# Optimization experiments

Measured on AMD Instinct MI355X. Metric: run time of the kernel, lower is better.

The kernel has to match this reference:

```python
import jax, jax.numpy as jnp
import numpy as np

N = 100000   # nodes
E = 625000   # edges
D = 128      # feature / embedding dim
C = 40       # num classes
BN_EPS = 1e-5
L2_EPS = 1e-12


def setup_inputs() -> dict:
    key = jax.random.key(0)
    ks = jax.random.split(key, 8)
    s = 1.0 / np.sqrt(D)
    return {
        "x": jax.random.normal(ks[0], (N, D), dtype=jnp.float32),
        "edge_index": jax.random.randint(ks[1], (2, E), 0, N, dtype=jnp.int64),
        "W1": jax.random.normal(ks[2], (D, D), dtype=jnp.float32) * s,
        "b1": jnp.zeros((D,), jnp.float32),
        "W2": jax.random.normal(ks[3], (D, D), dtype=jnp.float32) * s,
        "b2": jnp.zeros((D,), jnp.float32),
        "W3": jax.random.normal(ks[4], (D, D), dtype=jnp.float32) * s,
        "b3": jnp.zeros((D,), jnp.float32),
        "g1": jnp.ones((D,), jnp.float32), "be1": jnp.zeros((D,), jnp.float32),
        "g2": jnp.ones((D,), jnp.float32), "be2": jnp.zeros((D,), jnp.float32),
        "g3": jnp.ones((D,), jnp.float32), "be3": jnp.zeros((D,), jnp.float32),
        "Wout": jax.random.normal(ks[5], (D, C), dtype=jnp.float32) * s,
        "bout": jnp.zeros((C,), jnp.float32),
    }


def _gcn_norm(edge_index, n):
    # PyG GCNConv default: add self loops, symmetric normalization
    loop = jnp.arange(n)
    src = jnp.concatenate([edge_index[0], loop])
    dst = jnp.concatenate([edge_index[1], loop])
    deg = jax.ops.segment_sum(jnp.ones_like(src, dtype=jnp.float32), dst, num_segments=n)
    dinv = jnp.where(deg > 0, jax.lax.rsqrt(deg), 0.0)
    norm = dinv[src] * dinv[dst]  # [E+N]
    return src, dst, norm


def _gcn_conv(x, W, b, src, dst, norm, n):
    h = x @ W                                # [N, D]
    msg = h[src] * norm[:, None]             # gather, [E+N, D]
    out = jax.ops.segment_sum(msg, dst, num_segments=n)  # scatter-add
    return out + b


def _bn(x, g, b):
    mu = jnp.mean(x, axis=0)
    var = jnp.var(x, axis=0)
    return (x - mu) * jax.lax.rsqrt(var + BN_EPS) * g + b


def _l2norm(x):
    n = jnp.sqrt(jnp.sum(x * x, axis=1, keepdims=True))
    return x / jnp.maximum(n, L2_EPS)


def reference(x, edge_index, W1, b1, W2, b2, W3, b3,
              g1, be1, g2, be2, g3, be3, Wout, bout):
    n = x.shape[0]
    src, dst, norm = _gcn_norm(edge_index, n)

    h = jax.nn.relu(_bn(_gcn_conv(x, W1, b1, src, dst, norm, n), g1, be1))
    h = _l2norm(h)
    r = h
    h = jax.nn.relu(_bn(_gcn_conv(h, W2, b2, src, dst, norm, n), g2, be2))
    h = _l2norm(h + r)
    r = h
    h = jax.nn.relu(_bn(_gcn_conv(h, W3, b3, src, dst, norm, n), g3, be3))
    h = _l2norm(h + r)

    return h @ Wout + bout  # node classification logits [N, C]
```

## Files before the change

kernel.cpp:

```cpp
#include <hip/hip_runtime.h>
#include <math.h>

#define DD 128
#define COUT 40
#define BN_EPS 1e-5f
#define L2_EPS 1e-12f
#define NREP 64

typedef __attribute__((ext_vector_type(8))) short bf16x8;
typedef __attribute__((ext_vector_type(4))) float f32x4;

static __device__ inline unsigned short f2bf(float f) {
    unsigned int x = __float_as_uint(f);
    unsigned int r = (x + 0x7FFFu + ((x >> 16) & 1u)) >> 16;
    return (unsigned short)r;
}
static __device__ inline float bf2f(unsigned short u) {
    return __uint_as_float(((unsigned int)u) << 16);
}


__global__ void k_hist(const int* __restrict__ ei, int E, int* __restrict__ deg,
                       int* __restrict__ pord) {
    int i = blockIdx.x * blockDim.x + threadIdx.x;
    if (i < E) pord[i] = atomicAdd(&deg[ei[E + i]], 1);
}

__global__ void k_scan_a(const int* __restrict__ deg, int* __restrict__ row_ptr,
                         int* __restrict__ bsum, float* __restrict__ dinv, int n) {
    __shared__ int s[256];
    int t = threadIdx.x;
    int idx = blockIdx.x * 256 + t;
    int v = (idx < n) ? deg[idx] + 1 : 0;
    if (idx < n) dinv[idx] = rsqrtf((float)v);
    s[t] = v; __syncthreads();
    for (int off = 1; off < 256; off <<= 1) {
        int x = (t >= off) ? s[t - off] : 0;
        __syncthreads(); s[t] += x; __syncthreads();
    }
    if (idx <= n) row_ptr[idx] = s[t] - v;
    if (t == 255) bsum[blockIdx.x] = s[255];
}

__global__ void k_scan_b(const int* __restrict__ bsum, int* __restrict__ boff, int nb) {
    __shared__ int s[512];
    int t = threadIdx.x;
    int v = (t < nb) ? bsum[t] : 0;
    s[t] = v; __syncthreads();
    for (int off = 1; off < 512; off <<= 1) {
        int x = (t >= off) ? s[t - off] : 0;
        __syncthreads(); s[t] += x; __syncthreads();
    }
    if (t < nb) boff[t] = s[t] - v;
}

__global__ void k_scan_c(int* __restrict__ row_ptr, const int* __restrict__ boff, int n1) {
    int idx = blockIdx.x * blockDim.x + threadIdx.x;
    if (idx < n1) row_ptr[idx] += boff[idx >> 8];
}

__global__ void k_fill(const int* __restrict__ ei, const int* __restrict__ pord,
                       int E, int n, const int* __restrict__ row_ptr,
                       int* __restrict__ perm) {
    int i = blockIdx.x * blockDim.x + threadIdx.x;
    int total = E + n;
    if (i >= total) return;
    int u, pos;
    if (i < E) {
        u = ei[i];
        int v = ei[E + i];
        pos = row_ptr[v] + pord[i];
    } else {
        u = i - E;
        pos = row_ptr[u + 1] - 1;
    }
    perm[pos] = u;
}

__global__ void k_wrepack_all(const float* __restrict__ W1, const float* __restrict__ W2,
                              const float* __restrict__ W3, const float* __restrict__ Wout,
                              unsigned short* __restrict__ wb,
                              unsigned short* __restrict__ wob,
                              float* __restrict__ stats) {
    int b = blockIdx.x;
    if (b < 24) {
        int wi = b >> 3;
        const float* W = (wi == 0) ? W1 : (wi == 1) ? W2 : W3;
        unsigned short* out = wb + wi * 16384;
        int idx = (b & 7) * 256 + threadIdx.x;
        int kc = idx >> 9;
        int cc = (idx >> 6) & 7;
        int lane = idx & 63;
        int n = cc * 16 + (lane & 15);
        int kb = kc * 32 + (lane >> 4) * 8;
        unsigned short tmp[8];
#pragma unroll
        for (int j = 0; j < 8; j++) tmp[j] = f2bf(W[(size_t)(kb + j) * DD + n]);
        *(uint4*)&out[(size_t)idx * 8] = *(const uint4*)tmp;
    } else if (b < 27) {
        int idx = (b - 24) * 256 + threadIdx.x;
        int kc = idx / 192;
        int rem = idx % 192;
        int cc = rem >> 6;
        int lane = rem & 63;
        int n = cc * 16 + (lane & 15);
        int kb = kc * 32 + (lane >> 4) * 8;
        unsigned short tmp[8];
#pragma unroll
        for (int j = 0; j < 8; j++)
            tmp[j] = (n < COUT) ? f2bf(Wout[(size_t)(kb + j) * COUT + n]) : 0;
        *(uint4*)&wob[(size_t)idx * 8] = *(const uint4*)tmp;
    } else {
        float4 z = make_float4(0.f, 0.f, 0.f, 0.f);
        int idx = (b - 27) * 256 + threadIdx.x;
        for (int i = idx; i < 3 * NREP * 64; i += 8 * 256)
            ((float4*)stats)[i] = z;
    }
}


__global__ __launch_bounds__(256) void k_gemm0(const float* __restrict__ A,
                                               const unsigned short* __restrict__ Wb,
                                               const float* __restrict__ dinv,
                                               unsigned short* __restrict__ C, int nrows) {
    __shared__ __align__(16) unsigned short Ws[16384];
    const int tid = threadIdx.x;
    for (int i = tid; i < 2048; i += 256)
        ((uint4*)Ws)[i] = ((const uint4*)Wb)[i];
    __syncthreads();

    const int wv = tid >> 6;
    const int lane = tid & 63;
    const int R0 = blockIdx.x * 64 + wv * 16;
    if (R0 >= nrows) return;
    const int m = lane & 15, q = lane >> 4;
    int rr = R0 + m; if (rr >= nrows) rr = nrows - 1;
    const float* Ar = A + (size_t)rr * DD + q * 8;

    bf16x8 af[4];
#pragma unroll
    for (int kc = 0; kc < 4; kc++) {
        float4 lo = *(const float4*)(Ar + kc * 32);
        float4 hi = *(const float4*)(Ar + kc * 32 + 4);
        unsigned short t[8];
        t[0] = f2bf(lo.x); t[1] = f2bf(lo.y); t[2] = f2bf(lo.z); t[3] = f2bf(lo.w);
        t[4] = f2bf(hi.x); t[5] = f2bf(hi.y); t[6] = f2bf(hi.z); t[7] = f2bf(hi.w);
        af[kc] = *(const bf16x8*)t;
    }

    f32x4 acc[8];
#pragma unroll
    for (int cc = 0; cc < 8; cc++) acc[cc] = (f32x4){0.f, 0.f, 0.f, 0.f};
#pragma unroll
    for (int kc = 0; kc < 4; kc++)
#pragma unroll
        for (int cc = 0; cc < 8; cc++) {
            bf16x8 b = *(const bf16x8*)&Ws[(size_t)((kc * 8 + cc) * 64 + lane) * 8];
            acc[cc] = __builtin_amdgcn_mfma_f32_16x16x32_bf16(af[kc], b, acc[cc], 0, 0, 0);
        }

    float dr[4];
#pragma unroll
    for (int i = 0; i < 4; i++) {
        int r = R0 + q * 4 + i;
        dr[i] = (r < nrows) ? dinv[r] : 0.f;
    }
#pragma unroll
    for (int cc = 0; cc < 8; cc++)
#pragma unroll
        for (int i = 0; i < 4; i++) {
            int r = R0 + q * 4 + i;
            if (r < nrows) C[(size_t)r * DD + cc * 16 + m] = f2bf(acc[cc][i] * dr[i]);
        }
}

__global__ __launch_bounds__(256) void k_aggs(const unsigned short* __restrict__ lin,
                                              const int* __restrict__ row_ptr,
                                              const int* __restrict__ perm,
                                              const float* __restrict__ dinv,
                                              const float* __restrict__ bias,
                                              unsigned short* __restrict__ outb,
                                              float* __restrict__ stats, int n) {
    const int tid = threadIdx.x;
    const int wv = tid >> 6;
    const int lane = tid & 63;
    const int half = lane >> 5;
    const int li = lane & 31;
    const int slot = li >> 4;
    const int ci = (li & 15) * 8;

    const int v = blockIdx.x * 8 + wv * 2 + half;
    const bool valid = v < n;

    float acc[8];
#pragma unroll
    for (int k = 0; k < 8; k++) acc[k] = 0.f;
    float dv = 0.f;

    if (valid) {
        const int s0 = row_ptr[v];
        const int e0 = row_ptr[v + 1];
        dv = dinv[v];
        for (int j = s0; j < e0; j += 8) {
            int i0 = j + slot;
            int i1 = j + 2 + slot;
            int i2 = j + 4 + slot;
            int i3 = j + 6 + slot;
            bool b0 = i0 < e0, b1 = i1 < e0, b2 = i2 < e0, b3 = i3 < e0;
            int u0, u1, u2, u3;
            if (b0) u0 = perm[i0];
            if (b1) u1 = perm[i1];
            if (b2) u2 = perm[i2];
            if (b3) u3 = perm[i3];
            uint4 t0, t1, t2, t3;
            if (b0) t0 = *(const uint4*)&lin[(size_t)u0 * DD + ci];
            if (b1) t1 = *(const uint4*)&lin[(size_t)u1 * DD + ci];
            if (b2) t2 = *(const uint4*)&lin[(size_t)u2 * DD + ci];
            if (b3) t3 = *(const uint4*)&lin[(size_t)u3 * DD + ci];
            if (b0) {
                acc[0] += __uint_as_float(t0.x << 16);
                acc[1] += __uint_as_float(t0.x & 0xFFFF0000u);
                acc[2] += __uint_as_float(t0.y << 16);
                acc[3] += __uint_as_float(t0.y & 0xFFFF0000u);
                acc[4] += __uint_as_float(t0.z << 16);
                acc[5] += __uint_as_float(t0.z & 0xFFFF0000u);
                acc[6] += __uint_as_float(t0.w << 16);
                acc[7] += __uint_as_float(t0.w & 0xFFFF0000u);
            }
            if (b1) {
                acc[0] += __uint_as_float(t1.x << 16);
                acc[1] += __uint_as_float(t1.x & 0xFFFF0000u);
                acc[2] += __uint_as_float(t1.y << 16);
                acc[3] += __uint_as_float(t1.y & 0xFFFF0000u);
                acc[4] += __uint_as_float(t1.z << 16);
                acc[5] += __uint_as_float(t1.z & 0xFFFF0000u);
                acc[6] += __uint_as_float(t1.w << 16);
                acc[7] += __uint_as_float(t1.w & 0xFFFF0000u);
            }
            if (b2) {
                acc[0] += __uint_as_float(t2.x << 16);
                acc[1] += __uint_as_float(t2.x & 0xFFFF0000u);
                acc[2] += __uint_as_float(t2.y << 16);
                acc[3] += __uint_as_float(t2.y & 0xFFFF0000u);
                acc[4] += __uint_as_float(t2.z << 16);
                acc[5] += __uint_as_float(t2.z & 0xFFFF0000u);
                acc[6] += __uint_as_float(t2.w << 16);
                acc[7] += __uint_as_float(t2.w & 0xFFFF0000u);
            }
            if (b3) {
                acc[0] += __uint_as_float(t3.x << 16);
                acc[1] += __uint_as_float(t3.x & 0xFFFF0000u);
                acc[2] += __uint_as_float(t3.y << 16);
                acc[3] += __uint_as_float(t3.y & 0xFFFF0000u);
                acc[4] += __uint_as_float(t3.z << 16);
                acc[5] += __uint_as_float(t3.z & 0xFFFF0000u);
                acc[6] += __uint_as_float(t3.w << 16);
                acc[7] += __uint_as_float(t3.w & 0xFFFF0000u);
            }
        }
    }
#pragma unroll
    for (int k = 0; k < 8; k++) acc[k] += __shfl_xor(acc[k], 16, 64);

    __shared__ float sh[8][128];
    __shared__ float qh[8][128];
    const int prow = wv * 2 + half;
    if (slot == 0) {
        if (valid) {
            float4 bb0 = *(const float4*)&bias[ci];
            float4 bb1 = *(const float4*)&bias[ci + 4];
            float bs[8] = {bb0.x, bb0.y, bb0.z, bb0.w, bb1.x, bb1.y, bb1.z, bb1.w};
            unsigned short t[8];
#pragma unroll
            for (int k = 0; k < 8; k++) {
                float a = acc[k] * dv + bs[k];
                t[k] = f2bf(a);
                sh[prow][ci + k] = a;
                qh[prow][ci + k] = a * a;
            }
            *(uint4*)&outb[(size_t)v * DD + ci] = *(const uint4*)t;
        } else {
#pragma unroll
            for (int k = 0; k < 8; k++) { sh[prow][ci + k] = 0.f; qh[prow][ci + k] = 0.f; }
        }
    }
    __syncthreads();
    if (tid < 128) {
        float a = 0.f, b = 0.f;
#pragma unroll
        for (int g = 0; g < 8; g++) { a += sh[g][tid]; b += qh[g][tid]; }
        float* st = stats + (size_t)(blockIdx.x & (NREP - 1)) * 256;
        atomicAdd(&st[tid], a);
        atomicAdd(&st[128 + tid], b);
    }
}

template <bool HAS_RES>
__global__ __launch_bounds__(256) void k_fused(const unsigned short* __restrict__ aggX,
                                               const float* __restrict__ stats,
                                               const float* __restrict__ g,
                                               const float* __restrict__ be, float inv_n,
                                               const unsigned short* __restrict__ resb,
                                               const unsigned short* __restrict__ Wb,
                                               const float* __restrict__ dinv,
                                               unsigned short* __restrict__ hbf_out,
                                               unsigned short* __restrict__ linb_out,
                                               int nrows) {
    __shared__ __align__(16) unsigned short Ws[16384];
    __shared__ float ssl[256];
    const int tid = threadIdx.x;
    for (int i = tid; i < 2048; i += 256)
        ((uint4*)Ws)[i] = ((const uint4*)Wb)[i];
    if (tid < 128) {
        float sa = 0.f, sb = 0.f;
        for (int r = 0; r < NREP; r++) {
            sa += stats[r * 256 + tid];
            sb += stats[r * 256 + 128 + tid];
        }
        float mu = sa * inv_n;
        float var = sb * inv_n - mu * mu;
        float sc = g[tid] * rsqrtf(var + BN_EPS);
        ssl[tid] = sc;
        ssl[128 + tid] = be[tid] - mu * sc;
    }
    __syncthreads();

    const int wv = tid >> 6;
    const int lane = tid & 63;
    const int R0 = blockIdx.x * 64 + wv * 16;
    if (R0 >= nrows) return;
    const int m = lane & 15, q = lane >> 4;
    int rr = R0 + m; if (rr >= nrows) rr = nrows - 1;
    const unsigned short* Ar = aggX + (size_t)rr * DD + q * 8;
    const unsigned short* Rr = HAS_RES ? resb + (size_t)rr * DD + q * 8 : nullptr;

    float y[4][8];
    float sq = 0.f;
#pragma unroll
    for (int kc = 0; kc < 4; kc++) {
        ushort4 lo = *(const ushort4*)(Ar + kc * 32);
        ushort4 hi = *(const ushort4*)(Ar + kc * 32 + 4);
        unsigned short av[8] = {lo.x, lo.y, lo.z, lo.w, hi.x, hi.y, hi.z, hi.w};
        int c0 = kc * 32 + q * 8;
        float4 sc0 = *(const float4*)&ssl[c0];
        float4 sc1 = *(const float4*)&ssl[c0 + 4];
        float4 sh0 = *(const float4*)&ssl[128 + c0];
        float4 sh1 = *(const float4*)&ssl[128 + c0 + 4];
        float scv[8] = {sc0.x, sc0.y, sc0.z, sc0.w, sc1.x, sc1.y, sc1.z, sc1.w};
        float shv[8] = {sh0.x, sh0.y, sh0.z, sh0.w, sh1.x, sh1.y, sh1.z, sh1.w};
        if (HAS_RES) {
            ushort4 rl = *(const ushort4*)(Rr + kc * 32);
            ushort4 rh = *(const ushort4*)(Rr + kc * 32 + 4);
            unsigned short rv[8] = {rl.x, rl.y, rl.z, rl.w, rh.x, rh.y, rh.z, rh.w};
#pragma unroll
            for (int j = 0; j < 8; j++) {
                float yy = fmaxf(bf2f(av[j]) * scv[j] + shv[j], 0.f) + bf2f(rv[j]);
                y[kc][j] = yy; sq += yy * yy;
            }
        } else {
#pragma unroll
            for (int j = 0; j < 8; j++) {
                float yy = fmaxf(bf2f(av[j]) * scv[j] + shv[j], 0.f);
                y[kc][j] = yy; sq += yy * yy;
            }
        }
    }
    sq += __shfl_xor(sq, 16, 64);
    sq += __shfl_xor(sq, 32, 64);
    float inv = 1.f / fmaxf(sqrtf(sq), L2_EPS);

    bf16x8 af[4];
#pragma unroll
    for (int kc = 0; kc < 4; kc++) {
        unsigned short t[8];
#pragma unroll
        for (int j = 0; j < 8; j++) t[j] = f2bf(y[kc][j] * inv);
        af[kc] = *(const bf16x8*)t;
        *(bf16x8*)&hbf_out[(size_t)rr * DD + q * 8 + kc * 32] = af[kc];
    }

    f32x4 acc[8];
#pragma unroll
    for (int cc = 0; cc < 8; cc++) acc[cc] = (f32x4){0.f, 0.f, 0.f, 0.f};
#pragma unroll
    for (int kc = 0; kc < 4; kc++)
#pragma unroll
        for (int cc = 0; cc < 8; cc++) {
            bf16x8 b = *(const bf16x8*)&Ws[(size_t)((kc * 8 + cc) * 64 + lane) * 8];
            acc[cc] = __builtin_amdgcn_mfma_f32_16x16x32_bf16(af[kc], b, acc[cc], 0, 0, 0);
        }

    float dr[4];
#pragma unroll
    for (int i = 0; i < 4; i++) {
        int r = R0 + q * 4 + i;
        dr[i] = (r < nrows) ? dinv[r] : 0.f;
    }
#pragma unroll
    for (int cc = 0; cc < 8; cc++)
#pragma unroll
        for (int i = 0; i < 4; i++) {
            int r = R0 + q * 4 + i;
            if (r < nrows) linb_out[(size_t)r * DD + cc * 16 + m] = f2bf(acc[cc][i] * dr[i]);
        }
}

__global__ __launch_bounds__(256) void k_outfused(const unsigned short* __restrict__ aggX,
                                                  const float* __restrict__ stats,
                                                  const float* __restrict__ g,
                                                  const float* __restrict__ be, float inv_n,
                                                  const unsigned short* __restrict__ resb,
                                                  const unsigned short* __restrict__ wob,
                                                  const float* __restrict__ bout,
                                                  float* __restrict__ C, int nrows) {
    __shared__ __align__(16) unsigned short Ws[6144];
    __shared__ float ssl[256];
    const int tid = threadIdx.x;
    for (int i = tid; i < 768; i += 256)
        ((uint4*)Ws)[i] = ((const uint4*)wob)[i];
    if (tid < 128) {
        float sa = 0.f, sb = 0.f;
        for (int r = 0; r < NREP; r++) {
            sa += stats[r * 256 + tid];
            sb += stats[r * 256 + 128 + tid];
        }
        float mu = sa * inv_n;
        float var = sb * inv_n - mu * mu;
        float sc = g[tid] * rsqrtf(var + BN_EPS);
        ssl[tid] = sc;
        ssl[128 + tid] = be[tid] - mu * sc;
    }
    __syncthreads();

    const int wv = tid >> 6;
    const int lane = tid & 63;
    const int R0 = blockIdx.x * 64 + wv * 16;
    if (R0 >= nrows) return;
    const int m = lane & 15, q = lane >> 4;
    int rr = R0 + m; if (rr >= nrows) rr = nrows - 1;
    const unsigned short* Ar = aggX + (size_t)rr * DD + q * 8;
    const unsigned short* Rr = resb + (size_t)rr * DD + q * 8;

    float y[4][8];
    float sq = 0.f;
#pragma unroll
    for (int kc = 0; kc < 4; kc++) {
        ushort4 lo = *(const ushort4*)(Ar + kc * 32);
        ushort4 hi = *(const ushort4*)(Ar + kc * 32 + 4);
        ushort4 rl = *(const ushort4*)(Rr + kc * 32);
        ushort4 rh = *(const ushort4*)(Rr + kc * 32 + 4);
        unsigned short av[8] = {lo.x, lo.y, lo.z, lo.w, hi.x, hi.y, hi.z, hi.w};
        unsigned short rv[8] = {rl.x, rl.y, rl.z, rl.w, rh.x, rh.y, rh.z, rh.w};
        int c0 = kc * 32 + q * 8;
        float4 sc0 = *(const float4*)&ssl[c0];
        float4 sc1 = *(const float4*)&ssl[c0 + 4];
        float4 sh0 = *(const float4*)&ssl[128 + c0];
        float4 sh1 = *(const float4*)&ssl[128 + c0 + 4];
        float scv[8] = {sc0.x, sc0.y, sc0.z, sc0.w, sc1.x, sc1.y, sc1.z, sc1.w};
        float shv[8] = {sh0.x, sh0.y, sh0.z, sh0.w, sh1.x, sh1.y, sh1.z, sh1.w};
#pragma unroll
        for (int j = 0; j < 8; j++) {
            float yy = fmaxf(bf2f(av[j]) * scv[j] + shv[j], 0.f) + bf2f(rv[j]);
            y[kc][j] = yy; sq += yy * yy;
        }
    }
    sq += __shfl_xor(sq, 16, 64);
    sq += __shfl_xor(sq, 32, 64);
    float inv = 1.f / fmaxf(sqrtf(sq), L2_EPS);

    bf16x8 af[4];
#pragma unroll
    for (int kc = 0; kc < 4; kc++) {
        unsigned short t[8];
#pragma unroll
        for (int j = 0; j < 8; j++) t[j] = f2bf(y[kc][j] * inv);
        af[kc] = *(const bf16x8*)t;
    }

    f32x4 acc[3];
#pragma unroll
    for (int cc = 0; cc < 3; cc++) acc[cc] = (f32x4){0.f, 0.f, 0.f, 0.f};
#pragma unroll
    for (int kc = 0; kc < 4; kc++)
#pragma unroll
        for (int cc = 0; cc < 3; cc++) {
            bf16x8 b = *(const bf16x8*)&Ws[(size_t)((kc * 3 + cc) * 64 + lane) * 8];
            acc[cc] = __builtin_amdgcn_mfma_f32_16x16x32_bf16(af[kc], b, acc[cc], 0, 0, 0);
        }

#pragma unroll
    for (int cc = 0; cc < 3; cc++) {
        int col = cc * 16 + m;
        if (col < COUT) {
            float bb = bout[col];
#pragma unroll
            for (int i = 0; i < 4; i++) {
                int r = R0 + q * 4 + i;
                if (r < nrows) C[(size_t)r * COUT + col] = acc[cc][i] + bb;
            }
        }
    }
}


extern "C" void kernel_launch(void* const* d_in, const int* in_sizes, int n_in,
                              void* d_out, int out_size, void* d_ws, size_t ws_size,
                              hipStream_t stream) {
    const float* x    = (const float*)d_in[0];
    const int*   ei   = (const int*)d_in[1];
    const float* W1   = (const float*)d_in[2];
    const float* b1   = (const float*)d_in[3];
    const float* W2   = (const float*)d_in[4];
    const float* b2   = (const float*)d_in[5];
    const float* W3   = (const float*)d_in[6];
    const float* b3   = (const float*)d_in[7];
    const float* g1   = (const float*)d_in[8];
    const float* be1  = (const float*)d_in[9];
    const float* g2   = (const float*)d_in[10];
    const float* be2  = (const float*)d_in[11];
    const float* g3   = (const float*)d_in[12];
    const float* be3  = (const float*)d_in[13];
    const float* Wout = (const float*)d_in[14];
    const float* bout = (const float*)d_in[15];
    float* out = (float*)d_out;

    const int N = in_sizes[0] / DD;
    const int E = in_sizes[1] / 2;
    const int NNZ = E + N;
    const int SSTRIDE = NREP * 256;

    char* w = (char*)d_ws;
    unsigned short* linb = (unsigned short*)w; w += (size_t)N * DD * sizeof(unsigned short);
    unsigned short* aggA = (unsigned short*)w; w += (size_t)N * DD * sizeof(unsigned short);
    unsigned short* aggB = (unsigned short*)w; w += (size_t)N * DD * sizeof(unsigned short);
    unsigned short* hbf1 = (unsigned short*)w; w += (size_t)N * DD * sizeof(unsigned short);
    unsigned short* hbf2 = (unsigned short*)w; w += (size_t)N * DD * sizeof(unsigned short);
    unsigned short* wb   = (unsigned short*)w; w += 3 * 16384 * sizeof(unsigned short);
    unsigned short* wob  = (unsigned short*)w; w += 6144 * sizeof(unsigned short);
    int* perm    = (int*)w;                    w += (size_t)NNZ * sizeof(int);
    int* pord    = (int*)w;                    w += (size_t)E * sizeof(int);
    int* deg     = (int*)w;                    w += (size_t)N * sizeof(int);
    int* row_ptr = (int*)w;                    w += (size_t)(N + 1) * sizeof(int);
    float* dinv  = (float*)w;                  w += (size_t)N * sizeof(float);
    int* bsum    = (int*)w;                    w += 512 * sizeof(int);
    int* boff    = (int*)w;                    w += 512 * sizeof(int);
    float* stats = (float*)w;                  w += 3 * (size_t)SSTRIDE * sizeof(float);

    const int NB = (N + 1 + 255) / 256;

    hipMemsetAsync(deg, 0, (size_t)N * sizeof(int), stream);
    k_wrepack_all<<<35, 256, 0, stream>>>(W1, W2, W3, Wout, wb, wob, stats);
    k_hist<<<(E + 255) / 256, 256, 0, stream>>>(ei, E, deg, pord);
    k_scan_a<<<NB, 256, 0, stream>>>(deg, row_ptr, bsum, dinv, N);
    k_scan_b<<<1, 512, 0, stream>>>(bsum, boff, NB);
    k_scan_c<<<(N + 1 + 255) / 256, 256, 0, stream>>>(row_ptr, boff, N + 1);
    k_fill<<<(NNZ + 255) / 256, 256, 0, stream>>>(ei, pord, E, N, row_ptr, perm);

    int gemmGrid = (N + 63) / 64;
    int aggGrid = (N + 7) / 8;
    float inv_n = 1.0f / (float)N;

    k_gemm0<<<gemmGrid, 256, 0, stream>>>(x, wb, dinv, linb, N);
    k_aggs<<<aggGrid, 256, 0, stream>>>(linb, row_ptr, perm, dinv, b1, aggA, stats, N);
    k_fused<false><<<gemmGrid, 256, 0, stream>>>(aggA, stats, g1, be1, inv_n,
                                                 nullptr, wb + 16384, dinv, hbf1, linb, N);
    k_aggs<<<aggGrid, 256, 0, stream>>>(linb, row_ptr, perm, dinv, b2, aggB,
                                        stats + SSTRIDE, N);
    k_fused<true><<<gemmGrid, 256, 0, stream>>>(aggB, stats + SSTRIDE, g2, be2, inv_n,
                                                hbf1, wb + 32768, dinv, hbf2, linb, N);
    k_aggs<<<aggGrid, 256, 0, stream>>>(linb, row_ptr, perm, dinv, b3, aggA,
                                        stats + 2 * SSTRIDE, N);
    k_outfused<<<gemmGrid, 256, 0, stream>>>(aggA, stats + 2 * SSTRIDE, g3, be3, inv_n,
                                             hbf2, wob, bout, out, N);
}
```

Measured before the change: 404.5 us.

## Shard aggregation over feature columns with 16-lane groups per node

The SpMM aggregation kernel now splits the 128 feature columns into 8 shards handled by separate blocks. Each block covers 16 nodes, and each 16-lane group works on one node's 16-column slice, with 8 edge slots of 2 lanes each, reduced by shuffles. The aim is more parallelism per node and a simpler edge loop. In exchange, every block re-reads row_ptr and perm for its shard, and each gather is only 32 bytes per lane pair. Nontemporal loads and stores are also added for perm and the aggregation output.

```diff
diff --git a/kernel.cpp b/kernel.cpp
--- a/kernel.cpp
+++ b/kernel.cpp
@@ -9,6 +9,7 @@
 
 typedef __attribute__((ext_vector_type(8))) short bf16x8;
 typedef __attribute__((ext_vector_type(4))) float f32x4;
+typedef __attribute__((ext_vector_type(4))) unsigned int u32x4;
 
 static __device__ inline unsigned short f2bf(float f) {
     unsigned int x = __float_as_uint(f);
@@ -74,7 +75,7 @@
         u = i - E;
         pos = row_ptr[u + 1] - 1;
     }
-    perm[pos] = u;
+    __builtin_nontemporal_store(u, &perm[pos]);
 }
 
 __global__ void k_wrepack_all(const float* __restrict__ W1, const float* __restrict__ W2,
@@ -182,14 +183,15 @@
                                               unsigned short* __restrict__ outb,
                                               float* __restrict__ stats, int n) {
     const int tid = threadIdx.x;
-    const int wv = tid >> 6;
-    const int lane = tid & 63;
-    const int half = lane >> 5;
-    const int li = lane & 31;
-    const int slot = li >> 4;
-    const int ci = (li & 15) * 8;
-
-    const int v = blockIdx.x * 8 + wv * 2 + half;
+    const int shard = blockIdx.x & 7;
+    const int bg = blockIdx.x >> 3;
+    const int grp = tid >> 4;
+    const int li = tid & 15;
+    const int slot = li >> 1;
+    const int lp = li & 1;
+    const int c0 = shard * 16 + lp * 8;
+
+    const int v = bg * 16 + grp;
     const bool valid = v < n;
 
     float acc[8];
@@ -201,97 +203,56 @@
         const int s0 = row_ptr[v];
         const int e0 = row_ptr[v + 1];
         dv = dinv[v];
-        for (int j = s0; j < e0; j += 8) {
-            int i0 = j + slot;
-            int i1 = j + 2 + slot;
-            int i2 = j + 4 + slot;
-            int i3 = j + 6 + slot;
-            bool b0 = i0 < e0, b1 = i1 < e0, b2 = i2 < e0, b3 = i3 < e0;
-            int u0, u1, u2, u3;
-            if (b0) u0 = perm[i0];
-            if (b1) u1 = perm[i1];
-            if (b2) u2 = perm[i2];
-            if (b3) u3 = perm[i3];
-            uint4 t0, t1, t2, t3;
-            if (b0) t0 = *(const uint4*)&lin[(size_t)u0 * DD + ci];
-            if (b1) t1 = *(const uint4*)&lin[(size_t)u1 * DD + ci];
-            if (b2) t2 = *(const uint4*)&lin[(size_t)u2 * DD + ci];
-            if (b3) t3 = *(const uint4*)&lin[(size_t)u3 * DD + ci];
-            if (b0) {
-                acc[0] += __uint_as_float(t0.x << 16);
-                acc[1] += __uint_as_float(t0.x & 0xFFFF0000u);
-                acc[2] += __uint_as_float(t0.y << 16);
-                acc[3] += __uint_as_float(t0.y & 0xFFFF0000u);
-                acc[4] += __uint_as_float(t0.z << 16);
-                acc[5] += __uint_as_float(t0.z & 0xFFFF0000u);
-                acc[6] += __uint_as_float(t0.w << 16);
-                acc[7] += __uint_as_float(t0.w & 0xFFFF0000u);
-            }
-            if (b1) {
-                acc[0] += __uint_as_float(t1.x << 16);
-                acc[1] += __uint_as_float(t1.x & 0xFFFF0000u);
-                acc[2] += __uint_as_float(t1.y << 16);
-                acc[3] += __uint_as_float(t1.y & 0xFFFF0000u);
-                acc[4] += __uint_as_float(t1.z << 16);
-                acc[5] += __uint_as_float(t1.z & 0xFFFF0000u);
-                acc[6] += __uint_as_float(t1.w << 16);
-                acc[7] += __uint_as_float(t1.w & 0xFFFF0000u);
-            }
-            if (b2) {
-                acc[0] += __uint_as_float(t2.x << 16);
-                acc[1] += __uint_as_float(t2.x & 0xFFFF0000u);
-                acc[2] += __uint_as_float(t2.y << 16);
-                acc[3] += __uint_as_float(t2.y & 0xFFFF0000u);
-                acc[4] += __uint_as_float(t2.z << 16);
-                acc[5] += __uint_as_float(t2.z & 0xFFFF0000u);
-                acc[6] += __uint_as_float(t2.w << 16);
-                acc[7] += __uint_as_float(t2.w & 0xFFFF0000u);
-            }
-            if (b3) {
-                acc[0] += __uint_as_float(t3.x << 16);
-                acc[1] += __uint_as_float(t3.x & 0xFFFF0000u);
-                acc[2] += __uint_as_float(t3.y << 16);
-                acc[3] += __uint_as_float(t3.y & 0xFFFF0000u);
-                acc[4] += __uint_as_float(t3.z << 16);
-                acc[5] += __uint_as_float(t3.z & 0xFFFF0000u);
-                acc[6] += __uint_as_float(t3.w << 16);
-                acc[7] += __uint_as_float(t3.w & 0xFFFF0000u);
-            }
-        }
-    }
-#pragma unroll
-    for (int k = 0; k < 8; k++) acc[k] += __shfl_xor(acc[k], 16, 64);
-
-    __shared__ float sh[8][128];
-    __shared__ float qh[8][128];
-    const int prow = wv * 2 + half;
-    if (slot == 0) {
+        for (int j = s0 + slot; j < e0; j += 8) {
+            int u = __builtin_nontemporal_load(&perm[j]);
+            u32x4 t = *(const u32x4*)&lin[(size_t)u * DD + c0];
+            acc[0] += __uint_as_float(t[0] << 16);
+            acc[1] += __uint_as_float(t[0] & 0xFFFF0000u);
+            acc[2] += __uint_as_float(t[1] << 16);
+            acc[3] += __uint_as_float(t[1] & 0xFFFF0000u);
+            acc[4] += __uint_as_float(t[2] << 16);
+            acc[5] += __uint_as_float(t[2] & 0xFFFF0000u);
+            acc[6] += __uint_as_float(t[3] << 16);
+            acc[7] += __uint_as_float(t[3] & 0xFFFF0000u);
+        }
+    }
+#pragma unroll
+    for (int k = 0; k < 8; k++) {
+        acc[k] += __shfl_xor(acc[k], 2, 64);
+        acc[k] += __shfl_xor(acc[k], 4, 64);
+        acc[k] += __shfl_xor(acc[k], 8, 64);
+    }
+
+    __shared__ float sh[16][16];
+    __shared__ float qh[16][16];
+    if (li < 2) {
         if (valid) {
-            float4 bb0 = *(const float4*)&bias[ci];
-            float4 bb1 = *(const float4*)&bias[ci + 4];
+            float4 bb0 = *(const float4*)&bias[c0];
+            float4 bb1 = *(const float4*)&bias[c0 + 4];
             float bs[8] = {bb0.x, bb0.y, bb0.z, bb0.w, bb1.x, bb1.y, bb1.z, bb1.w};
             unsigned short t[8];
 #pragma unroll
             for (int k = 0; k < 8; k++) {
                 float a = acc[k] * dv + bs[k];
                 t[k] = f2bf(a);
-                sh[prow][ci + k] = a;
-                qh[prow][ci + k] = a * a;
+                sh[grp][lp * 8 + k] = a;
+                qh[grp][lp * 8 + k] = a * a;
             }
-            *(uint4*)&outb[(size_t)v * DD + ci] = *(const uint4*)t;
+            u32x4 tv = *(const u32x4*)t;
+            __builtin_nontemporal_store(tv, (u32x4*)&outb[(size_t)v * DD + c0]);
         } else {
 #pragma unroll
-            for (int k = 0; k < 8; k++) { sh[prow][ci + k] = 0.f; qh[prow][ci + k] = 0.f; }
+            for (int k = 0; k < 8; k++) { sh[grp][lp * 8 + k] = 0.f; qh[grp][lp * 8 + k] = 0.f; }
         }
     }
     __syncthreads();
-    if (tid < 128) {
+    if (tid < 16) {
         float a = 0.f, b = 0.f;
 #pragma unroll
-        for (int g = 0; g < 8; g++) { a += sh[g][tid]; b += qh[g][tid]; }
-        float* st = stats + (size_t)(blockIdx.x & (NREP - 1)) * 256;
-        atomicAdd(&st[tid], a);
-        atomicAdd(&st[128 + tid], b);
+        for (int g = 0; g < 16; g++) { a += sh[g][tid]; b += qh[g][tid]; }
+        float* st = stats + (size_t)((blockIdx.x >> 3) & (NREP - 1)) * 256;
+        atomicAdd(&st[shard * 16 + tid], a);
+        atomicAdd(&st[128 + shard * 16 + tid], b);
     }
 }
 
@@ -557,7 +518,7 @@
     k_fill<<<(NNZ + 255) / 256, 256, 0, stream>>>(ei, pord, E, N, row_ptr, perm);
 
     int gemmGrid = (N + 63) / 64;
-    int aggGrid = (N + 7) / 8;
+    int aggGrid = ((N + 15) / 16) * 8;
     float inv_n = 1.0f / (float)N;
 
     k_gemm0<<<gemmGrid, 256, 0, stream>>>(x, wb, dinv, linb, N);
```

Result: slower. 648.9 us (+60.4%).

## Overlap CSR graph construction with weight repack and first GEMM on a second stream

Applied to the files above, without the earlier changes.

Moves the degree histogram, prefix scan and CSR fill kernels onto a separate non-blocking stream, with events so the first GEMM waits only for dinv (after scan_a) and the first aggregation waits for the full CSR. The goal is to run graph preprocessing concurrently with weight repacking and the first feature GEMM instead of serially. It adds event and cross-stream synchronization overhead, and relies on statically created stream and event objects.

```diff
diff --git a/kernel.cpp b/kernel.cpp
--- a/kernel.cpp
+++ b/kernel.cpp
@@ -9,6 +9,7 @@
 
 typedef __attribute__((ext_vector_type(8))) short bf16x8;
 typedef __attribute__((ext_vector_type(4))) float f32x4;
+typedef __attribute__((ext_vector_type(4))) unsigned int u32x4;
 
 static __device__ inline unsigned short f2bf(float f) {
     unsigned int x = __float_as_uint(f);
@@ -17,6 +18,20 @@
 }
 static __device__ inline float bf2f(unsigned short u) {
     return __uint_as_float(((unsigned int)u) << 16);
+}
+
+namespace {
+struct AuxRes {
+    hipStream_t s2;
+    hipEvent_t evStart, evA, evF;
+    AuxRes() {
+        hipStreamCreateWithFlags(&s2, hipStreamNonBlocking);
+        hipEventCreateWithFlags(&evStart, hipEventDisableTiming);
+        hipEventCreateWithFlags(&evA, hipEventDisableTiming);
+        hipEventCreateWithFlags(&evF, hipEventDisableTiming);
+    }
+};
+AuxRes g_aux;
 }
 
 
@@ -548,19 +563,27 @@
 
     const int NB = (N + 1 + 255) / 256;
 
-    hipMemsetAsync(deg, 0, (size_t)N * sizeof(int), stream);
+    hipEventRecord(g_aux.evStart, stream);
+    hipStreamWaitEvent(g_aux.s2, g_aux.evStart, 0);
+
+    hipMemsetAsync(deg, 0, (size_t)N * sizeof(int), g_aux.s2);
+    k_hist<<<(E + 255) / 256, 256, 0, g_aux.s2>>>(ei, E, deg, pord);
+    k_scan_a<<<NB, 256, 0, g_aux.s2>>>(deg, row_ptr, bsum, dinv, N);
+    hipEventRecord(g_aux.evA, g_aux.s2);
+    k_scan_b<<<1, 512, 0, g_aux.s2>>>(bsum, boff, NB);
+    k_scan_c<<<(N + 1 + 255) / 256, 256, 0, g_aux.s2>>>(row_ptr, boff, N + 1);
+    k_fill<<<(NNZ + 255) / 256, 256, 0, g_aux.s2>>>(ei, pord, E, N, row_ptr, perm);
+    hipEventRecord(g_aux.evF, g_aux.s2);
+
     k_wrepack_all<<<35, 256, 0, stream>>>(W1, W2, W3, Wout, wb, wob, stats);
-    k_hist<<<(E + 255) / 256, 256, 0, stream>>>(ei, E, deg, pord);
-    k_scan_a<<<NB, 256, 0, stream>>>(deg, row_ptr, bsum, dinv, N);
-    k_scan_b<<<1, 512, 0, stream>>>(bsum, boff, NB);
-    k_scan_c<<<(N + 1 + 255) / 256, 256, 0, stream>>>(row_ptr, boff, N + 1);
-    k_fill<<<(NNZ + 255) / 256, 256, 0, stream>>>(ei, pord, E, N, row_ptr, perm);
 
     int gemmGrid = (N + 63) / 64;
     int aggGrid = (N + 7) / 8;
     float inv_n = 1.0f / (float)N;
 
+    hipStreamWaitEvent(stream, g_aux.evA, 0);
     k_gemm0<<<gemmGrid, 256, 0, stream>>>(x, wb, dinv, linb, N);
+    hipStreamWaitEvent(stream, g_aux.evF, 0);
     k_aggs<<<aggGrid, 256, 0, stream>>>(linb, row_ptr, perm, dinv, b1, aggA, stats, N);
     k_fused<false><<<gemmGrid, 256, 0, stream>>>(aggA, stats, g1, be1, inv_n,
                                                  nullptr, wb + 16384, dinv, hbf1, linb, N);
```

Measured after the change: 442.8 us. 9.5% more time.

## Drop self-loop CSR entries, fold block offsets into consumers, fuse deg zeroing

Applied to the files above, without the earlier changes.

Self-loops are no longer stored in the CSR. The aggregation kernel seeds its accumulator with the node's own row, and the degree count still adds one for the normalisation. The scan_c pass is removed: fill and aggregation add the per-block scan offset boff on the fly. The deg memset moves into the weight repack kernel. Together these remove two small launches and shrink the perm array, at the cost of an extra boff lookup per node in each aggregation.

```diff
diff --git a/kernel.cpp b/kernel.cpp
--- a/kernel.cpp
+++ b/kernel.cpp
@@ -9,6 +9,7 @@
 
 typedef __attribute__((ext_vector_type(8))) short bf16x8;
 typedef __attribute__((ext_vector_type(4))) float f32x4;
+typedef __attribute__((ext_vector_type(4))) unsigned int u32x4;
 
 static __device__ inline unsigned short f2bf(float f) {
     unsigned int x = __float_as_uint(f);
@@ -31,8 +32,8 @@
     __shared__ int s[256];
     int t = threadIdx.x;
     int idx = blockIdx.x * 256 + t;
-    int v = (idx < n) ? deg[idx] + 1 : 0;
-    if (idx < n) dinv[idx] = rsqrtf((float)v);
+    int v = (idx < n) ? deg[idx] : 0;
+    if (idx < n) dinv[idx] = rsqrtf((float)(v + 1));
     s[t] = v; __syncthreads();
     for (int off = 1; off < 256; off <<= 1) {
         int x = (t >= off) ? s[t - off] : 0;
@@ -54,26 +55,14 @@
     if (t < nb) boff[t] = s[t] - v;
 }
 
-__global__ void k_scan_c(int* __restrict__ row_ptr, const int* __restrict__ boff, int n1) {
-    int idx = blockIdx.x * blockDim.x + threadIdx.x;
-    if (idx < n1) row_ptr[idx] += boff[idx >> 8];
-}
-
 __global__ void k_fill(const int* __restrict__ ei, const int* __restrict__ pord,
-                       int E, int n, const int* __restrict__ row_ptr,
-                       int* __restrict__ perm) {
+                       int E, const int* __restrict__ row_ptr,
+                       const int* __restrict__ boff, int* __restrict__ perm) {
     int i = blockIdx.x * blockDim.x + threadIdx.x;
-    int total = E + n;
-    if (i >= total) return;
-    int u, pos;
-    if (i < E) {
-        u = ei[i];
-        int v = ei[E + i];
-        pos = row_ptr[v] + pord[i];
-    } else {
-        u = i - E;
-        pos = row_ptr[u + 1] - 1;
-    }
+    if (i >= E) return;
+    int u = ei[i];
+    int v = ei[E + i];
+    int pos = row_ptr[v] + boff[v >> 8] + pord[i];
     perm[pos] = u;
 }
 
@@ -81,7 +70,8 @@
                               const float* __restrict__ W3, const float* __restrict__ Wout,
                               unsigned short* __restrict__ wb,
                               unsigned short* __restrict__ wob,
-                              float* __restrict__ stats) {
+                              float* __restrict__ stats,
+                              int* __restrict__ deg, int n) {
     int b = blockIdx.x;
     if (b < 24) {
         int wi = b >> 3;
@@ -91,11 +81,11 @@
         int kc = idx >> 9;
         int cc = (idx >> 6) & 7;
         int lane = idx & 63;
-        int n = cc * 16 + (lane & 15);
+        int nn = cc * 16 + (lane & 15);
         int kb = kc * 32 + (lane >> 4) * 8;
         unsigned short tmp[8];
 #pragma unroll
-        for (int j = 0; j < 8; j++) tmp[j] = f2bf(W[(size_t)(kb + j) * DD + n]);
+        for (int j = 0; j < 8; j++) tmp[j] = f2bf(W[(size_t)(kb + j) * DD + nn]);
         *(uint4*)&out[(size_t)idx * 8] = *(const uint4*)tmp;
     } else if (b < 27) {
         int idx = (b - 24) * 256 + threadIdx.x;
@@ -103,18 +93,22 @@
         int rem = idx % 192;
         int cc = rem >> 6;
         int lane = rem & 63;
-        int n = cc * 16 + (lane & 15);
+        int nn = cc * 16 + (lane & 15);
         int kb = kc * 32 + (lane >> 4) * 8;
         unsigned short tmp[8];
 #pragma unroll
         for (int j = 0; j < 8; j++)
-            tmp[j] = (n < COUT) ? f2bf(Wout[(size_t)(kb + j) * COUT + n]) : 0;
+            tmp[j] = (nn < COUT) ? f2bf(Wout[(size_t)(kb + j) * COUT + nn]) : 0;
         *(uint4*)&wob[(size_t)idx * 8] = *(const uint4*)tmp;
     } else {
+        int idx = (b - 27) * 256 + threadIdx.x;
         float4 z = make_float4(0.f, 0.f, 0.f, 0.f);
-        int idx = (b - 27) * 256 + threadIdx.x;
         for (int i = idx; i < 3 * NREP * 64; i += 8 * 256)
             ((float4*)stats)[i] = z;
+        int4 iz = make_int4(0, 0, 0, 0);
+        for (int i = idx; i < (n >> 2); i += 8 * 256)
+            ((int4*)deg)[i] = iz;
+        if (b == 27 && threadIdx.x < (n & 3)) deg[(n & ~3) + threadIdx.x] = 0;
     }
 }
 
@@ -176,6 +170,7 @@
 
 __global__ __launch_bounds__(256) void k_aggs(const unsigned short* __restrict__ lin,
                                               const int* __restrict__ row_ptr,
+                                              const int* __restrict__ boff,
                                               const int* __restrict__ perm,
                                               const float* __restrict__ dinv,
                                               const float* __restrict__ bias,
@@ -198,9 +193,20 @@
     float dv = 0.f;
 
     if (valid) {
-        const int s0 = row_ptr[v];
-        const int e0 = row_ptr[v + 1];
+        const int s0 = row_ptr[v] + boff[v >> 8];
+        const int e0 = row_ptr[v + 1] + boff[(v + 1) >> 8];
         dv = dinv[v];
+        if (slot == 0) {
+            uint4 t = *(const uint4*)&lin[(size_t)v * DD + ci];
+            acc[0] = __uint_as_float(t.x << 16);
+            acc[1] = __uint_as_float(t.x & 0xFFFF0000u);
+            acc[2] = __uint_as_float(t.y << 16);
+            acc[3] = __uint_as_float(t.y & 0xFFFF0000u);
+            acc[4] = __uint_as_float(t.z << 16);
+            acc[5] = __uint_as_float(t.z & 0xFFFF0000u);
+            acc[6] = __uint_as_float(t.w << 16);
+            acc[7] = __uint_as_float(t.w & 0xFFFF0000u);
+        }
         for (int j = s0; j < e0; j += 8) {
             int i0 = j + slot;
             int i1 = j + 2 + slot;
@@ -526,7 +532,6 @@
 
     const int N = in_sizes[0] / DD;
     const int E = in_sizes[1] / 2;
-    const int NNZ = E + N;
     const int SSTRIDE = NREP * 256;
 
     char* w = (char*)d_ws;
@@ -537,7 +542,7 @@
     unsigned short* hbf2 = (unsigned short*)w; w += (size_t)N * DD * sizeof(unsigned short);
     unsigned short* wb   = (unsigned short*)w; w += 3 * 16384 * sizeof(unsigned short);
     unsigned short* wob  = (unsigned short*)w; w += 6144 * sizeof(unsigned short);
-    int* perm    = (int*)w;                    w += (size_t)NNZ * sizeof(int);
+    int* perm    = (int*)w;                    w += (size_t)E * sizeof(int);
     int* pord    = (int*)w;                    w += (size_t)E * sizeof(int);
     int* deg     = (int*)w;                    w += (size_t)N * sizeof(int);
     int* row_ptr = (int*)w;                    w += (size_t)(N + 1) * sizeof(int);
@@ -548,27 +553,25 @@
 
     const int NB = (N + 1 + 255) / 256;
 
-    hipMemsetAsync(deg, 0, (size_t)N * sizeof(int), stream);
-    k_wrepack_all<<<35, 256, 0, stream>>>(W1, W2, W3, Wout, wb, wob, stats);
+    k_wrepack_all<<<35, 256, 0, stream>>>(W1, W2, W3, Wout, wb, wob, stats, deg, N);
     k_hist<<<(E + 255) / 256, 256, 0, stream>>>(ei, E, deg, pord);
     k_scan_a<<<NB, 256, 0, stream>>>(deg, row_ptr, bsum, dinv, N);
     k_scan_b<<<1, 512, 0, stream>>>(bsum, boff, NB);
-    k_scan_c<<<(N + 1 + 255) / 256, 256, 0, stream>>>(row_ptr, boff, N + 1);
-    k_fill<<<(NNZ + 255) / 256, 256, 0, stream>>>(ei, pord, E, N, row_ptr, perm);
+    k_fill<<<(E + 255) / 256, 256, 0, stream>>>(ei, pord, E, row_ptr, boff, perm);
 
     int gemmGrid = (N + 63) / 64;
     int aggGrid = (N + 7) / 8;
     float inv_n = 1.0f / (float)N;
 
     k_gemm0<<<gemmGrid, 256, 0, stream>>>(x, wb, dinv, linb, N);
-    k_aggs<<<aggGrid, 256, 0, stream>>>(linb, row_ptr, perm, dinv, b1, aggA, stats, N);
+    k_aggs<<<aggGrid, 256, 0, stream>>>(linb, row_ptr, boff, perm, dinv, b1, aggA, stats, N);
     k_fused<false><<<gemmGrid, 256, 0, stream>>>(aggA, stats, g1, be1, inv_n,
                                                  nullptr, wb + 16384, dinv, hbf1, linb, N);
-    k_aggs<<<aggGrid, 256, 0, stream>>>(linb, row_ptr, perm, dinv, b2, aggB,
+    k_aggs<<<aggGrid, 256, 0, stream>>>(linb, row_ptr, boff, perm, dinv, b2, aggB,
                                         stats + SSTRIDE, N);
     k_fused<true><<<gemmGrid, 256, 0, stream>>>(aggB, stats + SSTRIDE, g2, be2, inv_n,
                                                 hbf1, wb + 32768, dinv, hbf2, linb, N);
-    k_aggs<<<aggGrid, 256, 0, stream>>>(linb, row_ptr, perm, dinv, b3, aggA,
+    k_aggs<<<aggGrid, 256, 0, stream>>>(linb, row_ptr, boff, perm, dinv, b3, aggA,
                                         stats + 2 * SSTRIDE, N);
     k_outfused<<<gemmGrid, 256, 0, stream>>>(aggA, stats + 2 * SSTRIDE, g3, be3, inv_n,
                                              hbf2, wob, bout, out, N);
```

New measurement: 395.6 us. -2.2%, faster.
